# Performance work log

Hardware: AMD Instinct MI355X
Metric: run time of the kernel (lower is better)

Reference implementation:

```python
import jax, jax.numpy as jnp
import numpy as np

B, CIN, HW = 32, 64, 56
K, KS, STRIDE, PAD = 128, 3, 1, 1


def setup_inputs() -> dict:
    key = jax.random.key(0)
    kx, kw, kb = jax.random.split(key, 3)
    x = jax.random.normal(kx, (B, CIN, HW, HW), dtype=jnp.float32)
    weight = jax.random.normal(kw, (K, CIN, KS, KS), dtype=jnp.float32)
    offset = jax.random.normal(kb, (K, 1, 1), dtype=jnp.float32)
    return {"x": x, "weight": weight, "offset": offset}


def reference(x, weight, offset):
    # conv2d (NCHW, OIHW) with stride/padding, then add per-kernel scalar offset.
    # Equivalent to the module's im2col (create_window_column_matrix) + matmul
    # + reshape, plus self.offset broadcast over (B, K, s, s).
    out = jax.lax.conv_general_dilated(
        x, weight,
        window_strides=(STRIDE, STRIDE),
        padding=[(PAD, PAD), (PAD, PAD)],
        dimension_numbers=("NCHW", "OIHW", "NCHW"),
    )
    return out + offset  # offset (K,1,1) broadcasts against (B,K,s,s)
```

## Files before the change

kernel.cpp:

```cpp
#include <hip/hip_runtime.h>
#include <hip/hip_bf16.h>

namespace {

using frag_t    = __attribute__((ext_vector_type(8))) short;
using f32x4     = __attribute__((ext_vector_type(4))) float;
using float4_t  = __attribute__((ext_vector_type(4))) float;

constexpr int BATCH = 32;
constexpr int CIN   = 64;
constexpr int HWD   = 56;
constexpr int KOUT  = 128;
constexpr int SP    = HWD * HWD;
constexpr int KD    = 9 * CIN;
constexpr int BN    = 128;
constexpr int HALO  = 57;
constexpr int WINR  = BN + 2 * HALO;
constexpr int NSTA  = 256;
constexpr int NT    = SP / BN + 1;
constexpr int NWG2  = NT * BATCH * 2;
constexpr int TT    = BATCH * (SP / 64);
constexpr int WB2   = (KOUT * KD) / 256;
constexpr int KHSTR = 18 * 2048;

__device__ inline unsigned short f2bf(float f) {
    __hip_bfloat16 h = __float2bfloat16(f);
    return __builtin_bit_cast(unsigned short, h);
}

__global__ __launch_bounds__(256)
void prep_kernel(const float* __restrict__ x, const float* __restrict__ w,
                 unsigned short* __restrict__ wpA2, unsigned short* __restrict__ xT)
{
    if (blockIdx.x >= TT) {
        const int idx = (blockIdx.x - TT) * 256 + threadIdx.x;
        const int q   = idx & 7;
        int r1 = idx >> 3;
        const int l  = r1 & 63;  r1 >>= 6;
        const int mi = r1 & 3;   r1 >>= 2;
        const int kc = r1 % 18;
        const int kh = r1 / 18;
        const int kout = kh * 64 + mi * 16 + (l & 15);
        const int kk   = kc * 32 + (l >> 4) * 8 + q;
        const int c = kk & 63, t = kk >> 6, ky = t / 3, kx = t - ky * 3;
        wpA2[idx] = f2bf(w[((kout * CIN + c) * 3 + ky) * 3 + kx]);
        return;
    }
    __shared__ float ls[64][68];
    const int bb   = blockIdx.x / (SP / 64);
    const int tile = blockIdx.x - bb * (SP / 64);
    const int sp0  = tile * 64;
    const int tid  = threadIdx.x;
    const int cq   = tid >> 4;
    const int spo  = (tid & 15) * 4;
    const float* xb = x + (size_t)bb * CIN * SP;
    #pragma unroll
    for (int j = 0; j < 4; ++j) {
        const int c = cq + 16 * j;
        float4_t v = *(const float4_t*)&xb[(size_t)c * SP + sp0 + spo];
        ls[spo + 0][c] = v.x; ls[spo + 1][c] = v.y;
        ls[spo + 2][c] = v.z; ls[spo + 3][c] = v.w;
    }
    __syncthreads();
    unsigned short* xo = xT + (size_t)(bb * SP + sp0) * 64;
    #pragma unroll
    for (int j = 0; j < 2; ++j) {
        const int s  = tid + 256 * j;
        const int sp = s >> 3, e = s & 7;
        frag_t u;
        #pragma unroll
        for (int q = 0; q < 8; ++q)
            u[q] = (short)f2bf(ls[sp][e * 8 + q]);
        *(frag_t*)&xo[sp * 64 + e * 8] = u;
    }
}

__global__ __launch_bounds__(256, 4)
void conv_areg(const unsigned short* __restrict__ xT, const unsigned short* __restrict__ wpA2,
               const float* __restrict__ off, float* __restrict__ out)
{
    __shared__ unsigned short xs[NSTA * 64];

    const int d    = blockIdx.x;
    const int wk   = (d & 7) * (NWG2 / 8) + (d >> 3);
    const int kh   = wk & 1;
    const int wk2  = wk >> 1;
    const int b    = wk2 / NT;
    const int sp0  = (wk2 - b * NT) * BN;
    const int tid  = threadIdx.x;
    const int lane = tid & 63;
    const int wid  = tid >> 6;

    {
        const unsigned short* xb = xT + (size_t)b * SP * 64;
        const int lsw = ((lane & 7) * 8) ^ ((lane >> 3) << 3);
        #pragma unroll
        for (int it = 0; it < 8; ++it) {
            const int R0 = it * 32 + wid * 8;
            const int r  = R0 + (lane >> 3);
            if (r < WINR) {
                int g = sp0 - HALO + r;
                g = min(max(g, 0), SP - 1);
                __builtin_amdgcn_global_load_lds(
                    (const __attribute__((address_space(1))) unsigned int*)
                        (xb + (size_t)g * 64 + lsw),
                    (__attribute__((address_space(3))) unsigned int*)
                        &xs[R0 * 64 + lane * 8],
                    16, 0, 0);
            }
        }
        *(unsigned int*)&xs[248 * 64 + tid * 2] = 0u;
    }
    asm volatile("s_waitcnt vmcnt(0)" ::: "memory");
    __syncthreads();

    const int l15 = lane & 15;
    const int l4  = lane >> 4;
    const int cread = 8 * l4;
    const int zaddr = 248 * 64 + cread;

    unsigned tm[9];
    int yv[8], xv[8];
    #pragma unroll
    for (int nf = 0; nf < 8; ++nf) {
        const int sp = sp0 + nf * 16 + l15;
        yv[nf] = sp / HWD;
        xv[nf] = sp - yv[nf] * HWD;
    }
    #pragma unroll
    for (int t = 0; t < 9; ++t) {
        const int dy = t / 3 - 1, dx = t % 3 - 1;
        unsigned m = 0;
        #pragma unroll
        for (int nf = 0; nf < 8; ++nf) {
            const bool v = ((unsigned)(yv[nf] + dy) < (unsigned)HWD) &
                           ((unsigned)(xv[nf] + dx) < (unsigned)HWD);
            m |= (v ? 1u : 0u) << nf;
        }
        tm[t] = m;
    }

    const unsigned short* ap = wpA2 + (size_t)kh * KHSTR + wid * 512 + lane * 8;

    f32x4 acc[8] = {};

    #pragma unroll
    for (int p = 0; p < 3; ++p) {
        frag_t aA[6];
        #pragma unroll
        for (int j = 0; j < 6; ++j)
            aA[j] = *(const frag_t*)(ap + (size_t)(p * 6 + j) * 2048);
        #pragma unroll
        for (int j = 0; j < 6; ++j) {
            const int kc = p * 6 + j;
            const int t  = kc >> 1;
            const int c0 = (kc & 1) * 32;
            const int shift = (t / 3 - 1) * HWD + (t % 3 - 1);
            const int row0b = l15 + HALO + shift;
            const int sw    = (row0b & 7) << 3;
            const int cadr  = (c0 + cread) ^ sw;
            const unsigned m = tm[t];
            frag_t bfr[8];
            #pragma unroll
            for (int nf = 0; nf < 8; ++nf) {
                const int ba = (row0b + 16 * nf) * 64 + cadr;
                const int ra = ((m >> nf) & 1u) ? ba : zaddr;
                bfr[nf] = *(const frag_t*)&xs[ra];
            }
            #pragma unroll
            for (int nf = 0; nf < 8; ++nf)
                acc[nf] = __builtin_amdgcn_mfma_f32_16x16x32_bf16(
                    aA[j], bfr[nf], acc[nf], 0, 0, 0);
        }
    }

    const int km0 = kh * 64 + wid * 16 + 4 * l4;
    const int spn = sp0 + l15;
    #pragma unroll
    for (int reg = 0; reg < 4; ++reg) {
        const int  kk  = km0 + reg;
        const float ofv = off[kk];
        float* ob = out + (size_t)(b * KOUT + kk) * SP;
        #pragma unroll
        for (int nf = 0; nf < 8; ++nf) {
            const int sp = spn + 16 * nf;
            if (sp < SP) ob[sp] = acc[nf][reg] + ofv;
        }
    }
}

__global__ __launch_bounds__(256)
void conv3x3_kernel(const float* __restrict__ x, const float* __restrict__ w,
                    const float* __restrict__ off, float* __restrict__ out)
{
    const int s  = blockIdx.x * 256 + threadIdx.x;
    const int b  = s / SP;
    const int sp = s - b * SP;
    const int y  = sp / HWD;
    const int xx = sp - y * HWD;
    const int k0 = blockIdx.y * 4;

    const int   xm1 = (xx > 0) ? xx - 1 : 0;
    const int   xp1 = (xx < HWD - 1) ? xx + 1 : HWD - 1;
    const float m0  = (xx > 0) ? 1.f : 0.f;
    const float m2  = (xx < HWD - 1) ? 1.f : 0.f;

    int ro[3]; float msk[3][3];
    #pragma unroll
    for (int ky = 0; ky < 3; ++ky) {
        const int  yy = y + ky - 1;
        const bool ok = (unsigned)yy < (unsigned)HWD;
        const float rm = ok ? 1.f : 0.f;
        ro[ky] = (ok ? yy : 0) * HWD;
        msk[ky][0] = rm * m0; msk[ky][1] = rm; msk[ky][2] = rm * m2;
    }
    float acc[4] = {0.f, 0.f, 0.f, 0.f};
    const float* xb = x + (size_t)b * CIN * SP;
    for (int c = 0; c < CIN; ++c) {
        const float* xc = xb + (size_t)c * SP;
        #pragma unroll
        for (int ky = 0; ky < 3; ++ky) {
            const float* xr = xc + ro[ky];
            const float v0 = xr[xm1] * msk[ky][0];
            const float v1 = xr[xx]  * msk[ky][1];
            const float v2 = xr[xp1] * msk[ky][2];
            const int wi = c * 9 + ky * 3;
            #pragma unroll
            for (int kk = 0; kk < 4; ++kk) {
                const float* wr = w + (size_t)(k0 + kk) * (CIN * 9) + wi;
                acc[kk] = fmaf(v0, wr[0], acc[kk]);
                acc[kk] = fmaf(v1, wr[1], acc[kk]);
                acc[kk] = fmaf(v2, wr[2], acc[kk]);
            }
        }
    }
    #pragma unroll
    for (int kk = 0; kk < 4; ++kk)
        out[(size_t)(b * KOUT + k0 + kk) * SP + sp] = acc[kk] + off[k0 + kk];
}

}

extern "C" void kernel_launch(void* const* d_in, const int* in_sizes, int n_in,
                              void* d_out, int out_size, void* d_ws, size_t ws_size,
                              hipStream_t stream)
{
    const float* x   = (const float*)d_in[0];
    const float* w   = (const float*)d_in[1];
    const float* off = (const float*)d_in[2];
    float* out = (float*)d_out;

    const size_t wpa_bytes = (size_t)KOUT * KD * 2;
    const size_t xt_bytes  = (size_t)BATCH * SP * CIN * 2;

    if (ws_size >= wpa_bytes + xt_bytes) {
        unsigned short* wpA2 = (unsigned short*)d_ws;
        unsigned short* xT   = (unsigned short*)((char*)d_ws + wpa_bytes);
        prep_kernel<<<TT + WB2, 256, 0, stream>>>(x, w, wpA2, xT);
        conv_areg<<<NWG2, dim3(256, 1, 1), 0, stream>>>(xT, wpA2, off, out);
    } else {
        dim3 grid((BATCH * SP) / 256, KOUT / 4);
        conv3x3_kernel<<<grid, dim3(256, 1, 1), 0, stream>>>(x, w, off, out);
    }
}
```

Before: 40.76 us.

## Retile conv to 64-pixel blocks covering all 128 output channels per workgroup

Each workgroup now covers 64 spatial positions and all 128 output channels, so each wave computes 32 channels times 64 pixels, instead of half the channels over 128 pixels. This removes the duplicated staging of the same input window into LDS by two workgroups (one per channel half) and drops the padded partial tile, since 3136 divides evenly by 64. The halo window shrinks to 192 rows, giving a higher halo-to-useful ratio per tile. Each wave now loads twice as many A fragments, but the grid keeps roughly the same number of workgroups.

```diff
diff --git a/kernel.cpp b/kernel.cpp
--- a/kernel.cpp
+++ b/kernel.cpp
@@ -13,12 +13,12 @@
 constexpr int KOUT  = 128;
 constexpr int SP    = HWD * HWD;
 constexpr int KD    = 9 * CIN;
-constexpr int BN    = 128;
+constexpr int BN    = 64;
 constexpr int HALO  = 57;
 constexpr int WINR  = BN + 2 * HALO;
-constexpr int NSTA  = 256;
-constexpr int NT    = SP / BN + 1;
-constexpr int NWG2  = NT * BATCH * 2;
+constexpr int NSTA  = 192;
+constexpr int NT    = SP / BN;
+constexpr int NWG   = NT * BATCH;
 constexpr int TT    = BATCH * (SP / 64);
 constexpr int WB2   = (KOUT * KD) / 256;
 constexpr int KHSTR = 18 * 2048;
@@ -76,17 +76,15 @@
 }
 
 __global__ __launch_bounds__(256, 4)
-void conv_areg(const unsigned short* __restrict__ xT, const unsigned short* __restrict__ wpA2,
-               const float* __restrict__ off, float* __restrict__ out)
+void conv_b2(const unsigned short* __restrict__ xT, const unsigned short* __restrict__ wpA2,
+             const float* __restrict__ off, float* __restrict__ out)
 {
     __shared__ unsigned short xs[NSTA * 64];
 
     const int d    = blockIdx.x;
-    const int wk   = (d & 7) * (NWG2 / 8) + (d >> 3);
-    const int kh   = wk & 1;
-    const int wk2  = wk >> 1;
-    const int b    = wk2 / NT;
-    const int sp0  = (wk2 - b * NT) * BN;
+    const int wk   = (d & 7) * (NWG / 8) + (d >> 3);
+    const int b    = wk / NT;
+    const int sp0  = (wk - b * NT) * BN;
     const int tid  = threadIdx.x;
     const int lane = tid & 63;
     const int wid  = tid >> 6;
@@ -95,7 +93,7 @@
         const unsigned short* xb = xT + (size_t)b * SP * 64;
         const int lsw = ((lane & 7) * 8) ^ ((lane >> 3) << 3);
         #pragma unroll
-        for (int it = 0; it < 8; ++it) {
+        for (int it = 0; it < 6; ++it) {
             const int R0 = it * 32 + wid * 8;
             const int r  = R0 + (lane >> 3);
             if (r < WINR) {
@@ -109,7 +107,7 @@
                     16, 0, 0);
             }
         }
-        *(unsigned int*)&xs[248 * 64 + tid * 2] = 0u;
+        *(unsigned int*)&xs[184 * 64 + tid * 2] = 0u;
     }
     asm volatile("s_waitcnt vmcnt(0)" ::: "memory");
     __syncthreads();
@@ -117,12 +115,12 @@
     const int l15 = lane & 15;
     const int l4  = lane >> 4;
     const int cread = 8 * l4;
-    const int zaddr = 248 * 64 + cread;
-
-    unsigned tm[9];
-    int yv[8], xv[8];
-    #pragma unroll
-    for (int nf = 0; nf < 8; ++nf) {
+    const int zaddr = 184 * 64 + cread;
+
+    unsigned long long mbits = 0ull;
+    int yv[4], xv[4];
+    #pragma unroll
+    for (int nf = 0; nf < 4; ++nf) {
         const int sp = sp0 + nf * 16 + l15;
         yv[nf] = sp / HWD;
         xv[nf] = sp - yv[nf] * HWD;
@@ -130,61 +128,65 @@
     #pragma unroll
     for (int t = 0; t < 9; ++t) {
         const int dy = t / 3 - 1, dx = t % 3 - 1;
-        unsigned m = 0;
-        #pragma unroll
-        for (int nf = 0; nf < 8; ++nf) {
+        #pragma unroll
+        for (int nf = 0; nf < 4; ++nf) {
             const bool v = ((unsigned)(yv[nf] + dy) < (unsigned)HWD) &
                            ((unsigned)(xv[nf] + dx) < (unsigned)HWD);
-            m |= (v ? 1u : 0u) << nf;
-        }
-        tm[t] = m;
-    }
-
-    const unsigned short* ap = wpA2 + (size_t)kh * KHSTR + wid * 512 + lane * 8;
-
-    f32x4 acc[8] = {};
-
-    #pragma unroll
-    for (int p = 0; p < 3; ++p) {
-        frag_t aA[6];
-        #pragma unroll
-        for (int j = 0; j < 6; ++j)
-            aA[j] = *(const frag_t*)(ap + (size_t)(p * 6 + j) * 2048);
-        #pragma unroll
-        for (int j = 0; j < 6; ++j) {
-            const int kc = p * 6 + j;
+            mbits |= (unsigned long long)(v ? 1 : 0) << (t * 4 + nf);
+        }
+    }
+
+    const unsigned short* ap = wpA2 + (size_t)(wid >> 1) * KHSTR
+                                    + (wid & 1) * 1024 + lane * 8;
+    const frag_t zf = {0,0,0,0,0,0,0,0};
+    f32x4 acc[2][4] = {};
+
+    #pragma unroll
+    for (int p = 0; p < 6; ++p) {
+        frag_t aB[6];
+        #pragma unroll
+        for (int j = 0; j < 3; ++j)
+            #pragma unroll
+            for (int m = 0; m < 2; ++m)
+                aB[j * 2 + m] = *(const frag_t*)(ap + (size_t)(p * 3 + j) * 2048 + m * 512);
+        #pragma unroll
+        for (int j = 0; j < 3; ++j) {
+            const int kc = p * 3 + j;
             const int t  = kc >> 1;
             const int c0 = (kc & 1) * 32;
             const int shift = (t / 3 - 1) * HWD + (t % 3 - 1);
             const int row0b = l15 + HALO + shift;
             const int sw    = (row0b & 7) << 3;
             const int cadr  = (c0 + cread) ^ sw;
-            const unsigned m = tm[t];
-            frag_t bfr[8];
-            #pragma unroll
-            for (int nf = 0; nf < 8; ++nf) {
+            const unsigned m4 = (unsigned)((mbits >> (t * 4)) & 15ull);
+            frag_t bfr[4];
+            #pragma unroll
+            for (int nf = 0; nf < 4; ++nf) {
                 const int ba = (row0b + 16 * nf) * 64 + cadr;
-                const int ra = ((m >> nf) & 1u) ? ba : zaddr;
+                const int ra = ((m4 >> nf) & 1u) ? ba : zaddr;
                 bfr[nf] = *(const frag_t*)&xs[ra];
             }
             #pragma unroll
-            for (int nf = 0; nf < 8; ++nf)
-                acc[nf] = __builtin_amdgcn_mfma_f32_16x16x32_bf16(
-                    aA[j], bfr[nf], acc[nf], 0, 0, 0);
-        }
-    }
-
-    const int km0 = kh * 64 + wid * 16 + 4 * l4;
+            for (int m = 0; m < 2; ++m)
+                #pragma unroll
+                for (int nf = 0; nf < 4; ++nf)
+                    acc[m][nf] = __builtin_amdgcn_mfma_f32_16x16x32_bf16(
+                        aB[j * 2 + m], bfr[nf], acc[m][nf], 0, 0, 0);
+        }
+    }
+
     const int spn = sp0 + l15;
     #pragma unroll
-    for (int reg = 0; reg < 4; ++reg) {
-        const int  kk  = km0 + reg;
-        const float ofv = off[kk];
-        float* ob = out + (size_t)(b * KOUT + kk) * SP;
-        #pragma unroll
-        for (int nf = 0; nf < 8; ++nf) {
-            const int sp = spn + 16 * nf;
-            if (sp < SP) ob[sp] = acc[nf][reg] + ofv;
+    for (int m = 0; m < 2; ++m) {
+        const int km = wid * 32 + m * 16 + 4 * l4;
+        #pragma unroll
+        for (int reg = 0; reg < 4; ++reg) {
+            const int  kk  = km + reg;
+            const float ofv = off[kk];
+            float* ob = out + (size_t)(b * KOUT + kk) * SP;
+            #pragma unroll
+            for (int nf = 0; nf < 4; ++nf)
+                ob[spn + 16 * nf] = acc[m][nf][reg] + ofv;
         }
     }
 }
@@ -257,7 +259,7 @@
         unsigned short* wpA2 = (unsigned short*)d_ws;
         unsigned short* xT   = (unsigned short*)((char*)d_ws + wpa_bytes);
         prep_kernel<<<TT + WB2, 256, 0, stream>>>(x, w, wpA2, xT);
-        conv_areg<<<NWG2, dim3(256, 1, 1), 0, stream>>>(xT, wpA2, off, out);
+        conv_b2<<<NWG, dim3(256, 1, 1), 0, stream>>>(xT, wpA2, off, out);
     } else {
         dim3 grid((BATCH * SP) / 256, KOUT / 4);
         conv3x3_kernel<<<grid, dim3(256, 1, 1), 0, stream>>>(x, w, off, out);
```

After: 40.13 us. No clear change (-1.5%).
